# Optimization experiments

Measured on AMD Instinct MI355X. Metric: run time of the kernel, lower is better.

The kernel has to match this reference:

```python
import jax, jax.numpy as jnp
import numpy as np

B, H, SQ, SKV, D, TOPK = 1, 16, 1024, 4096, 128, 64


def setup_inputs() -> dict:
    key = jax.random.key(0)
    kq, kk, kv, ki, ks = jax.random.split(key, 5)
    q = jax.random.normal(kq, (B, H, SQ, D), dtype=jnp.float32)
    k = jax.random.normal(kk, (B, H, SKV, D), dtype=jnp.float32)
    v = jax.random.normal(kv, (B, H, SKV, D), dtype=jnp.float32)
    topk_indices = jax.random.randint(ki, (B, SQ, TOPK), 0, SKV, dtype=jnp.int32)
    topk_scores = jax.random.uniform(ks, (B, SQ, TOPK), dtype=jnp.float32)
    return {"q": q, "k": k, "v": v, "topk_indices": topk_indices,
            "topk_scores": topk_scores}


def reference(q, k, v, topk_indices, topk_scores):
    # q: (b,h,s,d); k,v: (b,h,S,d) global (cp_world_size=1 all-gather is identity)
    head_dim = q.shape[-1]
    scale = head_dim ** -0.5
    # Gather selected K/V per query without dense (b,h,s,S,d) expansion.
    # idx: (b,1,s,topk,1) broadcast against (b,h,1,S,d) along axis=3.
    idx = topk_indices[:, None, :, :, None]
    k_g = jnp.take_along_axis(k[:, :, None, :, :], idx, axis=3)  # (b,h,s,t,d)
    v_g = jnp.take_along_axis(v[:, :, None, :, :], idx, axis=3)  # (b,h,s,t,d)
    scores = jnp.einsum("bhsd,bhstd->bhst", q, k_g) * scale
    w = jax.nn.softmax(scores, axis=-1)
    # rescale by indexer scores and renormalize
    w = w * topk_scores[:, None, :, :]
    w = w / (jnp.sum(w, axis=-1, keepdims=True) + 1e-12)
    out = jnp.einsum("bhst,bhstd->bhsd", w, v_g)
    return out
```

## Files before the change

kernel.cpp:

```cpp
#include <hip/hip_runtime.h>

#define NH  16
#define SQL 1024
#define SKV 4096
#define HD  128
#define TK  64

__device__ __forceinline__ float blo(unsigned u) { return __uint_as_float(u << 16); }
__device__ __forceinline__ float bhi(unsigned u) { return __uint_as_float(u & 0xFFFF0000u); }

__global__ __launch_bounds__(256) void cvt_bf16(const float* __restrict__ src,
                                                unsigned short* __restrict__ dst,
                                                int n8) {
    int i = blockIdx.x * 256 + threadIdx.x;
    if (i >= n8) return;
    const float4* s4 = (const float4*)src;
    float4 a = s4[2 * i], b = s4[2 * i + 1];
    float f[8] = {a.x, a.y, a.z, a.w, b.x, b.y, b.z, b.w};
    unsigned r[8];
#pragma unroll
    for (int j = 0; j < 8; ++j) {
        unsigned u = __float_as_uint(f[j]);
        r[j] = (u + 0x7FFFu + ((u >> 16) & 1u)) >> 16;
    }
    uint4 o;
    o.x = r[0] | (r[1] << 16);
    o.y = r[2] | (r[3] << 16);
    o.z = r[4] | (r[5] << 16);
    o.w = r[6] | (r[7] << 16);
    ((uint4*)dst)[i] = o;
}

__global__ __launch_bounds__(256) void dsa_bf16(
    const float* __restrict__ q, const unsigned short* __restrict__ kb16,
    const unsigned short* __restrict__ vb16, const int* __restrict__ tidx,
    const float* __restrict__ tsc, float* __restrict__ out)
{
    __shared__ int   idxs[4][TK];
    __shared__ float wsc[4][TK];

    const int tid  = threadIdx.x;
    const int wv   = tid >> 6;
    const int lane = tid & 63;
    const int quad = lane >> 4;
    const int l16  = lane & 15;
    const int bi   = blockIdx.x;

    const int h = ((bi >> 11) << 3) | (bi & 7);
    const int s = (((bi >> 3) & 255) << 2) + wv;

    const float* qp = q + (size_t)(h * SQL + s) * HD + 8 * l16;
    const float4 qa = *(const float4*)qp;
    const float4 qb = *(const float4*)(qp + 4);

    idxs[wv][lane] = tidx[s * TK + lane];
    const float t_sc = tsc[s * TK + lane];

    const unsigned short* kb = kb16 + (size_t)h * SKV * HD;
#pragma unroll 8
    for (int i = 0; i < TK / 4; ++i) {
        const int t   = 4 * i + quad;
        const int row = idxs[wv][t];
        uint4 kw = *(const uint4*)(kb + (size_t)row * HD + 8 * l16);
        float d;
        d  = qa.x * blo(kw.x) + qa.y * bhi(kw.x);
        d += qa.z * blo(kw.y) + qa.w * bhi(kw.y);
        d += qb.x * blo(kw.z) + qb.y * bhi(kw.z);
        d += qb.z * blo(kw.w) + qb.w * bhi(kw.w);
        d += __shfl_xor(d, 8);
        d += __shfl_xor(d, 4);
        d += __shfl_xor(d, 2);
        d += __shfl_xor(d, 1);
        if (l16 == 0) wsc[wv][t] = d;
    }

    float acc = wsc[wv][lane] * 0.08838834764831845f;
    float m = acc;
#pragma unroll
    for (int off = 32; off; off >>= 1) m = fmaxf(m, __shfl_xor(m, off));
    const float e   = __expf(acc - m);
    const float ets = e * t_sc;
    float se = e, sets = ets;
#pragma unroll
    for (int off = 32; off; off >>= 1) {
        se   += __shfl_xor(se, off);
        sets += __shfl_xor(sets, off);
    }
    wsc[wv][lane] = ets / (sets + 1e-12f * se);

    const unsigned short* vb = vb16 + (size_t)h * SKV * HD;
    float o[8] = {0.f, 0.f, 0.f, 0.f, 0.f, 0.f, 0.f, 0.f};
#pragma unroll 8
    for (int i = 0; i < TK / 4; ++i) {
        const int t    = 4 * i + quad;
        const int row  = idxs[wv][t];
        const float wt = wsc[wv][t];
        uint4 vw = *(const uint4*)(vb + (size_t)row * HD + 8 * l16);
        o[0] += wt * blo(vw.x);  o[1] += wt * bhi(vw.x);
        o[2] += wt * blo(vw.y);  o[3] += wt * bhi(vw.y);
        o[4] += wt * blo(vw.z);  o[5] += wt * bhi(vw.z);
        o[6] += wt * blo(vw.w);  o[7] += wt * bhi(vw.w);
    }
#pragma unroll
    for (int j = 0; j < 8; ++j) {
        o[j] += __shfl_xor(o[j], 16);
        o[j] += __shfl_xor(o[j], 32);
    }
    if (quad == 0) {
        float* op = out + (size_t)(h * SQL + s) * HD + 8 * l16;
        *(float4*)op       = make_float4(o[0], o[1], o[2], o[3]);
        *(float4*)(op + 4) = make_float4(o[4], o[5], o[6], o[7]);
    }
}

__global__ __launch_bounds__(256) void dsa_fp32(
    const float* __restrict__ q, const float* __restrict__ k,
    const float* __restrict__ v, const int* __restrict__ tidx,
    const float* __restrict__ tsc, float* __restrict__ out)
{
    __shared__ int   idxs[4][TK];
    __shared__ float wsc[4][TK];
    const int tid = threadIdx.x, wv = tid >> 6, lane = tid & 63;
    const int half = lane >> 5, l32 = lane & 31, bi = blockIdx.x;
    const int h = ((bi & 7) << 1) | ((bi >> 3) & 1);
    const int s = ((bi >> 4) << 2) + wv;
    const float* qp = q + (size_t)(h * SQL + s) * HD;
    const float4 qf = *(const float4*)(qp + 4 * l32);
    const float t_sc = tsc[s * TK + lane];
    idxs[wv][lane] = tidx[s * TK + lane];
    const float* kb = k + (size_t)h * SKV * HD;
#pragma unroll 4
    for (int i = 0; i < TK / 2; ++i) {
        const int t = 2 * i + half, row = idxs[wv][t];
        float4 k4 = *(const float4*)(kb + (size_t)row * HD + 4 * l32);
        float d = k4.x * qf.x + k4.y * qf.y + k4.z * qf.z + k4.w * qf.w;
        d += __shfl_xor(d, 16); d += __shfl_xor(d, 8); d += __shfl_xor(d, 4);
        d += __shfl_xor(d, 2);  d += __shfl_xor(d, 1);
        if (l32 == 0) wsc[wv][t] = d;
    }
    float acc = wsc[wv][lane] * 0.08838834764831845f;
    float m = acc;
#pragma unroll
    for (int off = 32; off; off >>= 1) m = fmaxf(m, __shfl_xor(m, off));
    const float e = __expf(acc - m), ets = e * t_sc;
    float se = e, sets = ets;
#pragma unroll
    for (int off = 32; off; off >>= 1) { se += __shfl_xor(se, off); sets += __shfl_xor(sets, off); }
    wsc[wv][lane] = ets / (sets + 1e-12f * se);
    const float* vbp = v + (size_t)h * SKV * HD;
    float4 o = make_float4(0.f, 0.f, 0.f, 0.f);
#pragma unroll 4
    for (int i = 0; i < TK / 2; ++i) {
        const int t = 2 * i + half, row = idxs[wv][t];
        const float wt = wsc[wv][t];
        float4 v4 = *(const float4*)(vbp + (size_t)row * HD + 4 * l32);
        o.x += wt * v4.x; o.y += wt * v4.y; o.z += wt * v4.z; o.w += wt * v4.w;
    }
    o.x += __shfl_xor(o.x, 32); o.y += __shfl_xor(o.y, 32);
    o.z += __shfl_xor(o.z, 32); o.w += __shfl_xor(o.w, 32);
    if (half == 0) *(float4*)(out + (size_t)(h * SQL + s) * HD + 4 * l32) = o;
}

extern "C" void kernel_launch(void* const* d_in, const int* in_sizes, int n_in,
                              void* d_out, int out_size, void* d_ws, size_t ws_size,
                              hipStream_t stream) {
    const float* q  = (const float*)d_in[0];
    const float* k  = (const float*)d_in[1];
    const float* v  = (const float*)d_in[2];
    const int*   ti = (const int*)d_in[3];
    const float* ts = (const float*)d_in[4];
    float* out = (float*)d_out;

    const size_t nkv  = (size_t)NH * SKV * HD;
    const size_t need = 2 * nkv * sizeof(unsigned short);
    if (ws_size >= need) {
        unsigned short* kb16 = (unsigned short*)d_ws;
        unsigned short* vb16 = kb16 + nkv;
        const int n8 = (int)(nkv / 8);
        cvt_bf16<<<dim3(n8 / 256), dim3(256), 0, stream>>>(k, kb16, n8);
        cvt_bf16<<<dim3(n8 / 256), dim3(256), 0, stream>>>(v, vb16, n8);
        dsa_bf16<<<dim3(4096), dim3(256), 0, stream>>>(q, kb16, vb16, ti, ts, out);
    } else {
        dsa_fp32<<<dim3(4096), dim3(256), 0, stream>>>(q, k, v, ti, ts, out);
    }
}
```

Baseline: 144.4 us.

## Transpose bf16 K/V to token-major layout and process all heads per query

The bf16 conversion now writes K and V in a [token][head][dim] layout, and one fused conversion kernel replaces the two separate ones. The attention kernel assigns one block per query position, covering all 16 heads. For each selected index, the 16 heads' rows then form one contiguous 4KB chunk rather than 16 scattered 256B reads, and the index and score loads are shared across heads. The cost is fewer blocks (1024), a more serial loop of 64 steps per lane, and a strided transposed write during conversion.

```diff
diff --git a/kernel.cpp b/kernel.cpp
--- a/kernel.cpp
+++ b/kernel.cpp
@@ -9,59 +9,70 @@
 __device__ __forceinline__ float blo(unsigned u) { return __uint_as_float(u << 16); }
 __device__ __forceinline__ float bhi(unsigned u) { return __uint_as_float(u & 0xFFFF0000u); }
 
-__global__ __launch_bounds__(256) void cvt_bf16(const float* __restrict__ src,
-                                                unsigned short* __restrict__ dst,
-                                                int n8) {
-    int i = blockIdx.x * 256 + threadIdx.x;
-    if (i >= n8) return;
-    const float4* s4 = (const float4*)src;
-    float4 a = s4[2 * i], b = s4[2 * i + 1];
-    float f[8] = {a.x, a.y, a.z, a.w, b.x, b.y, b.z, b.w};
-    unsigned r[8];
-#pragma unroll
-    for (int j = 0; j < 8; ++j) {
-        unsigned u = __float_as_uint(f[j]);
-        r[j] = (u + 0x7FFFu + ((u >> 16) & 1u)) >> 16;
-    }
-    uint4 o;
-    o.x = r[0] | (r[1] << 16);
-    o.y = r[2] | (r[3] << 16);
-    o.z = r[4] | (r[5] << 16);
-    o.w = r[6] | (r[7] << 16);
-    ((uint4*)dst)[i] = o;
+__device__ __forceinline__ unsigned bfpack2(float x, float y) {
+    unsigned ux = __float_as_uint(x), uy = __float_as_uint(y);
+    ux = (ux + 0x7FFFu + ((ux >> 16) & 1u)) >> 16;
+    uy = (uy + 0x7FFFu + ((uy >> 16) & 1u)) & 0xFFFF0000u;
+    return ux | uy;
 }
 
-__global__ __launch_bounds__(256) void dsa_bf16(
-    const float* __restrict__ q, const unsigned short* __restrict__ kb16,
-    const unsigned short* __restrict__ vb16, const int* __restrict__ tidx,
+__global__ __launch_bounds__(256) void cvt_hsi(
+    const float* __restrict__ k, const float* __restrict__ v,
+    unsigned short* __restrict__ kt, unsigned short* __restrict__ vt)
+{
+    int b = blockIdx.x;
+    const float* src;
+    unsigned short* dst;
+    if (b < 4096) { src = k; dst = kt; }
+    else          { src = v; dst = vt; b -= 4096; }
+    const int h  = b & 15;
+    const int i  = ((b >> 4) << 4) + (threadIdx.x >> 4);
+    const int c  = threadIdx.x & 15;
+
+    const float* sp = src + ((size_t)h * SKV + i) * HD + c * 8;
+    float4 a = *(const float4*)sp;
+    float4 d = *(const float4*)(sp + 4);
+    uint4 o;
+    o.x = bfpack2(a.x, a.y);
+    o.y = bfpack2(a.z, a.w);
+    o.z = bfpack2(d.x, d.y);
+    o.w = bfpack2(d.z, d.w);
+    *(uint4*)(dst + ((size_t)i * NH + h) * HD + c * 8) = o;
+}
+
+__global__ __launch_bounds__(256) void dsa_hsi(
+    const float* __restrict__ q, const unsigned short* __restrict__ kt,
+    const unsigned short* __restrict__ vt, const int* __restrict__ tidx,
     const float* __restrict__ tsc, float* __restrict__ out)
 {
-    __shared__ int   idxs[4][TK];
-    __shared__ float wsc[4][TK];
+    __shared__ int   idxs[TK];
+    __shared__ float tscs[TK];
+    __shared__ float wsc[NH][TK + 1];
 
     const int tid  = threadIdx.x;
+    const int lane = tid & 63;
     const int wv   = tid >> 6;
-    const int lane = tid & 63;
-    const int quad = lane >> 4;
-    const int l16  = lane & 15;
-    const int bi   = blockIdx.x;
+    const int c    = lane & 15;
+    const int h    = (wv << 2) | (lane >> 4);
+    const int s    = blockIdx.x;
 
-    const int h = ((bi >> 11) << 3) | (bi & 7);
-    const int s = (((bi >> 3) & 255) << 2) + wv;
+    if (tid < TK) {
+        idxs[tid] = tidx[s * TK + tid];
+        tscs[tid] = tsc[s * TK + tid];
+    }
 
-    const float* qp = q + (size_t)(h * SQL + s) * HD + 8 * l16;
+    const float* qp = q + ((size_t)h * SQL + s) * HD + c * 8;
     const float4 qa = *(const float4*)qp;
     const float4 qb = *(const float4*)(qp + 4);
 
-    idxs[wv][lane] = tidx[s * TK + lane];
-    const float t_sc = tsc[s * TK + lane];
+    __syncthreads();
+    const float myts = tscs[lane];
 
-    const unsigned short* kb = kb16 + (size_t)h * SKV * HD;
+    const unsigned short* kbase = kt + h * HD + c * 8;
 #pragma unroll 8
-    for (int i = 0; i < TK / 4; ++i) {
-        const int t   = 4 * i + quad;
-        const int row = idxs[wv][t];
-        uint4 kw = *(const uint4*)(kb + (size_t)row * HD + 8 * l16);
+    for (int t = 0; t < TK; ++t) {
+        const size_t row = (size_t)idxs[t];
+        uint4 kw = *(const uint4*)(kbase + (row << 11));
         float d;
         d  = qa.x * blo(kw.x) + qa.y * bhi(kw.x);
         d += qa.z * blo(kw.y) + qa.w * bhi(kw.y);
@@ -71,46 +82,43 @@
         d += __shfl_xor(d, 4);
         d += __shfl_xor(d, 2);
         d += __shfl_xor(d, 1);
-        if (l16 == 0) wsc[wv][t] = d;
+        if (c == 0) wsc[h][t] = d;
     }
 
-    float acc = wsc[wv][lane] * 0.08838834764831845f;
-    float m = acc;
 #pragma unroll
-    for (int off = 32; off; off >>= 1) m = fmaxf(m, __shfl_xor(m, off));
-    const float e   = __expf(acc - m);
-    const float ets = e * t_sc;
-    float se = e, sets = ets;
+    for (int hh = 0; hh < 4; ++hh) {
+        const int hx = (wv << 2) | hh;
+        float a = wsc[hx][lane] * 0.08838834764831845f;
+        float m = a;
 #pragma unroll
-    for (int off = 32; off; off >>= 1) {
-        se   += __shfl_xor(se, off);
-        sets += __shfl_xor(sets, off);
+        for (int off = 32; off; off >>= 1) m = fmaxf(m, __shfl_xor(m, off));
+        const float e   = __expf(a - m);
+        const float ets = e * myts;
+        float se = e, sets = ets;
+#pragma unroll
+        for (int off = 32; off; off >>= 1) {
+            se   += __shfl_xor(se, off);
+            sets += __shfl_xor(sets, off);
+        }
+        wsc[hx][lane] = ets / (sets + 1e-12f * se);
     }
-    wsc[wv][lane] = ets / (sets + 1e-12f * se);
 
-    const unsigned short* vb = vb16 + (size_t)h * SKV * HD;
-    float o[8] = {0.f, 0.f, 0.f, 0.f, 0.f, 0.f, 0.f, 0.f};
+    const unsigned short* vbase = vt + h * HD + c * 8;
+    float o0=0.f,o1=0.f,o2=0.f,o3=0.f,o4=0.f,o5=0.f,o6=0.f,o7=0.f;
 #pragma unroll 8
-    for (int i = 0; i < TK / 4; ++i) {
-        const int t    = 4 * i + quad;
-        const int row  = idxs[wv][t];
-        const float wt = wsc[wv][t];
-        uint4 vw = *(const uint4*)(vb + (size_t)row * HD + 8 * l16);
-        o[0] += wt * blo(vw.x);  o[1] += wt * bhi(vw.x);
-        o[2] += wt * blo(vw.y);  o[3] += wt * bhi(vw.y);
-        o[4] += wt * blo(vw.z);  o[5] += wt * bhi(vw.z);
-        o[6] += wt * blo(vw.w);  o[7] += wt * bhi(vw.w);
+    for (int t = 0; t < TK; ++t) {
+        const size_t row = (size_t)idxs[t];
+        const float  wt  = wsc[h][t];
+        uint4 vw = *(const uint4*)(vbase + (row << 11));
+        o0 += wt * blo(vw.x);  o1 += wt * bhi(vw.x);
+        o2 += wt * blo(vw.y);  o3 += wt * bhi(vw.y);
+        o4 += wt * blo(vw.z);  o5 += wt * bhi(vw.z);
+        o6 += wt * blo(vw.w);  o7 += wt * bhi(vw.w);
     }
-#pragma unroll
-    for (int j = 0; j < 8; ++j) {
-        o[j] += __shfl_xor(o[j], 16);
-        o[j] += __shfl_xor(o[j], 32);
-    }
-    if (quad == 0) {
-        float* op = out + (size_t)(h * SQL + s) * HD + 8 * l16;
-        *(float4*)op       = make_float4(o[0], o[1], o[2], o[3]);
-        *(float4*)(op + 4) = make_float4(o[4], o[5], o[6], o[7]);
-    }
+
+    float* op = out + ((size_t)h * SQL + s) * HD + c * 8;
+    *(float4*)op       = make_float4(o0, o1, o2, o3);
+    *(float4*)(op + 4) = make_float4(o4, o5, o6, o7);
 }
 
 __global__ __launch_bounds__(256) void dsa_fp32(
@@ -174,12 +182,10 @@
     const size_t nkv  = (size_t)NH * SKV * HD;
     const size_t need = 2 * nkv * sizeof(unsigned short);
     if (ws_size >= need) {
-        unsigned short* kb16 = (unsigned short*)d_ws;
-        unsigned short* vb16 = kb16 + nkv;
-        const int n8 = (int)(nkv / 8);
-        cvt_bf16<<<dim3(n8 / 256), dim3(256), 0, stream>>>(k, kb16, n8);
-        cvt_bf16<<<dim3(n8 / 256), dim3(256), 0, stream>>>(v, vb16, n8);
-        dsa_bf16<<<dim3(4096), dim3(256), 0, stream>>>(q, kb16, vb16, ti, ts, out);
+        unsigned short* kt = (unsigned short*)d_ws;
+        unsigned short* vt = kt + nkv;
+        cvt_hsi<<<dim3(8192), dim3(256), 0, stream>>>(k, v, kt, vt);
+        dsa_hsi<<<dim3(SQL), dim3(256), 0, stream>>>(q, kt, vt, ti, ts, out);
     } else {
         dsa_fp32<<<dim3(4096), dim3(256), 0, stream>>>(q, k, v, ti, ts, out);
     }
```

New measurement: 175.0 us. 21.2% more time.

## Switch K/V staging from bf16 to fp16 with packed dot and hfma2 math

Applied to the files above, without the earlier changes.

Converts K and V to fp16 instead of bf16 in one merged conversion kernel, removing one launch. The QK dot product now uses packed fp16 fdot2 with fp32 accumulation, and the PV accumulation uses packed half2 FMAs with half-precision accumulators and shuffles. This cuts the ALU work spent unpacking bf16 and doing scalar FMAs. The cost is lower precision: fp16 accumulation of the output risks rounding error, and overflow for large inputs, compared with the fp32 reference.

```diff
diff --git a/kernel.cpp b/kernel.cpp
--- a/kernel.cpp
+++ b/kernel.cpp
@@ -1,4 +1,5 @@
 #include <hip/hip_runtime.h>
+#include <hip/hip_fp16.h>
 
 #define NH  16
 #define SQL 1024
@@ -6,34 +7,35 @@
 #define HD  128
 #define TK  64
 
-__device__ __forceinline__ float blo(unsigned u) { return __uint_as_float(u << 16); }
-__device__ __forceinline__ float bhi(unsigned u) { return __uint_as_float(u & 0xFFFF0000u); }
-
-__global__ __launch_bounds__(256) void cvt_bf16(const float* __restrict__ src,
-                                                unsigned short* __restrict__ dst,
-                                                int n8) {
-    int i = blockIdx.x * 256 + threadIdx.x;
-    if (i >= n8) return;
+typedef _Float16 h2_t __attribute__((ext_vector_type(2)));
+
+__device__ __forceinline__ unsigned pkh(float x, float y) {
+    return (unsigned)__half_as_ushort(__float2half(x)) |
+           ((unsigned)__half_as_ushort(__float2half(y)) << 16);
+}
+
+__global__ __launch_bounds__(256) void cvt_f16(
+    const float* __restrict__ k, const float* __restrict__ v,
+    unsigned short* __restrict__ kh, unsigned short* __restrict__ vh)
+{
+    int b = blockIdx.x;
+    const float* src; unsigned short* dst;
+    if (b < 4096) { src = k; dst = kh; }
+    else          { src = v; dst = vh; b -= 4096; }
+    const size_t i = (size_t)b * 256 + threadIdx.x;
     const float4* s4 = (const float4*)src;
-    float4 a = s4[2 * i], b = s4[2 * i + 1];
-    float f[8] = {a.x, a.y, a.z, a.w, b.x, b.y, b.z, b.w};
-    unsigned r[8];
-#pragma unroll
-    for (int j = 0; j < 8; ++j) {
-        unsigned u = __float_as_uint(f[j]);
-        r[j] = (u + 0x7FFFu + ((u >> 16) & 1u)) >> 16;
-    }
+    float4 a = s4[2 * i], c = s4[2 * i + 1];
     uint4 o;
-    o.x = r[0] | (r[1] << 16);
-    o.y = r[2] | (r[3] << 16);
-    o.z = r[4] | (r[5] << 16);
-    o.w = r[6] | (r[7] << 16);
+    o.x = pkh(a.x, a.y);
+    o.y = pkh(a.z, a.w);
+    o.z = pkh(c.x, c.y);
+    o.w = pkh(c.z, c.w);
     ((uint4*)dst)[i] = o;
 }
 
-__global__ __launch_bounds__(256) void dsa_bf16(
-    const float* __restrict__ q, const unsigned short* __restrict__ kb16,
-    const unsigned short* __restrict__ vb16, const int* __restrict__ tidx,
+__global__ __launch_bounds__(256) void dsa_f16(
+    const float* __restrict__ q, const unsigned short* __restrict__ kh,
+    const unsigned short* __restrict__ vh, const int* __restrict__ tidx,
     const float* __restrict__ tsc, float* __restrict__ out)
 {
     __shared__ int   idxs[4][TK];
@@ -52,21 +54,36 @@
     const float* qp = q + (size_t)(h * SQL + s) * HD + 8 * l16;
     const float4 qa = *(const float4*)qp;
     const float4 qb = *(const float4*)(qp + 4);
+    h2_t q0 = {(_Float16)qa.x, (_Float16)qa.y};
+    h2_t q1 = {(_Float16)qa.z, (_Float16)qa.w};
+    h2_t q2 = {(_Float16)qb.x, (_Float16)qb.y};
+    h2_t q3 = {(_Float16)qb.z, (_Float16)qb.w};
 
     idxs[wv][lane] = tidx[s * TK + lane];
     const float t_sc = tsc[s * TK + lane];
 
-    const unsigned short* kb = kb16 + (size_t)h * SKV * HD;
+    const unsigned short* kb = kh + (size_t)h * SKV * HD;
 #pragma unroll 8
     for (int i = 0; i < TK / 4; ++i) {
         const int t   = 4 * i + quad;
-        const int row = idxs[wv][t];
-        uint4 kw = *(const uint4*)(kb + (size_t)row * HD + 8 * l16);
-        float d;
-        d  = qa.x * blo(kw.x) + qa.y * bhi(kw.x);
-        d += qa.z * blo(kw.y) + qa.w * bhi(kw.y);
-        d += qb.x * blo(kw.z) + qb.y * bhi(kw.z);
-        d += qb.z * blo(kw.w) + qb.w * bhi(kw.w);
+        const size_t row = (size_t)idxs[wv][t];
+        uint4 kw = *(const uint4*)(kb + row * HD + 8 * l16);
+        float d = 0.f;
+#if __has_builtin(__builtin_amdgcn_fdot2)
+        d = __builtin_amdgcn_fdot2(q0, __builtin_bit_cast(h2_t, kw.x), d, false);
+        d = __builtin_amdgcn_fdot2(q1, __builtin_bit_cast(h2_t, kw.y), d, false);
+        d = __builtin_amdgcn_fdot2(q2, __builtin_bit_cast(h2_t, kw.z), d, false);
+        d = __builtin_amdgcn_fdot2(q3, __builtin_bit_cast(h2_t, kw.w), d, false);
+#else
+        {
+            float2 k0 = __half22float2(__builtin_bit_cast(__half2, kw.x));
+            float2 k1 = __half22float2(__builtin_bit_cast(__half2, kw.y));
+            float2 k2 = __half22float2(__builtin_bit_cast(__half2, kw.z));
+            float2 k3 = __half22float2(__builtin_bit_cast(__half2, kw.w));
+            d  = qa.x * k0.x + qa.y * k0.y + qa.z * k1.x + qa.w * k1.y;
+            d += qb.x * k2.x + qb.y * k2.y + qb.z * k3.x + qb.w * k3.y;
+        }
+#endif
         d += __shfl_xor(d, 8);
         d += __shfl_xor(d, 4);
         d += __shfl_xor(d, 2);
@@ -88,28 +105,38 @@
     }
     wsc[wv][lane] = ets / (sets + 1e-12f * se);
 
-    const unsigned short* vb = vb16 + (size_t)h * SKV * HD;
-    float o[8] = {0.f, 0.f, 0.f, 0.f, 0.f, 0.f, 0.f, 0.f};
+    const unsigned short* vb = vh + (size_t)h * SKV * HD;
+    __half2 o0 = __float2half2_rn(0.f);
+    __half2 o1 = o0, o2 = o0, o3 = o0;
 #pragma unroll 8
     for (int i = 0; i < TK / 4; ++i) {
         const int t    = 4 * i + quad;
-        const int row  = idxs[wv][t];
-        const float wt = wsc[wv][t];
-        uint4 vw = *(const uint4*)(vb + (size_t)row * HD + 8 * l16);
-        o[0] += wt * blo(vw.x);  o[1] += wt * bhi(vw.x);
-        o[2] += wt * blo(vw.y);  o[3] += wt * bhi(vw.y);
-        o[4] += wt * blo(vw.z);  o[5] += wt * bhi(vw.z);
-        o[6] += wt * blo(vw.w);  o[7] += wt * bhi(vw.w);
-    }
-#pragma unroll
-    for (int j = 0; j < 8; ++j) {
-        o[j] += __shfl_xor(o[j], 16);
-        o[j] += __shfl_xor(o[j], 32);
-    }
+        const size_t row = (size_t)idxs[wv][t];
+        const __half2 w2 = __float2half2_rn(wsc[wv][t]);
+        uint4 vw = *(const uint4*)(vb + row * HD + 8 * l16);
+        o0 = __hfma2(w2, __builtin_bit_cast(__half2, vw.x), o0);
+        o1 = __hfma2(w2, __builtin_bit_cast(__half2, vw.y), o1);
+        o2 = __hfma2(w2, __builtin_bit_cast(__half2, vw.z), o2);
+        o3 = __hfma2(w2, __builtin_bit_cast(__half2, vw.w), o3);
+    }
+
+    __half2 oo[4] = {o0, o1, o2, o3};
+#pragma unroll
+    for (int j = 0; j < 4; ++j) {
+        unsigned u = __builtin_bit_cast(unsigned, oo[j]);
+        oo[j] = __hadd2(oo[j], __builtin_bit_cast(__half2, __shfl_xor(u, 16)));
+        u = __builtin_bit_cast(unsigned, oo[j]);
+        oo[j] = __hadd2(oo[j], __builtin_bit_cast(__half2, __shfl_xor(u, 32)));
+    }
+
     if (quad == 0) {
+        float2 f0 = __half22float2(oo[0]);
+        float2 f1 = __half22float2(oo[1]);
+        float2 f2 = __half22float2(oo[2]);
+        float2 f3 = __half22float2(oo[3]);
         float* op = out + (size_t)(h * SQL + s) * HD + 8 * l16;
-        *(float4*)op       = make_float4(o[0], o[1], o[2], o[3]);
-        *(float4*)(op + 4) = make_float4(o[4], o[5], o[6], o[7]);
+        *(float4*)op       = make_float4(f0.x, f0.y, f1.x, f1.y);
+        *(float4*)(op + 4) = make_float4(f2.x, f2.y, f3.x, f3.y);
     }
 }
 
@@ -174,12 +201,10 @@
     const size_t nkv  = (size_t)NH * SKV * HD;
     const size_t need = 2 * nkv * sizeof(unsigned short);
     if (ws_size >= need) {
-        unsigned short* kb16 = (unsigned short*)d_ws;
-        unsigned short* vb16 = kb16 + nkv;
-        const int n8 = (int)(nkv / 8);
-        cvt_bf16<<<dim3(n8 / 256), dim3(256), 0, stream>>>(k, kb16, n8);
-        cvt_bf16<<<dim3(n8 / 256), dim3(256), 0, stream>>>(v, vb16, n8);
-        dsa_bf16<<<dim3(4096), dim3(256), 0, stream>>>(q, kb16, vb16, ti, ts, out);
+        unsigned short* kh = (unsigned short*)d_ws;
+        unsigned short* vh = kh + nkv;
+        cvt_f16<<<dim3(8192), dim3(256), 0, stream>>>(k, v, kh, vh);
+        dsa_f16<<<dim3(4096), dim3(256), 0, stream>>>(q, kh, vh, ti, ts, out);
     } else {
         dsa_fp32<<<dim3(4096), dim3(256), 0, stream>>>(q, k, v, ti, ts, out);
     }
```

Result: no change. 142.8 us (-1.1%).
